# Kernel tuning notes

Measured on AMD Instinct MI355X. Metric: run time of the kernel, lower is better.

The kernel has to match this reference:

```python
import jax, jax.numpy as jnp
import numpy as np

B, L, D = 32, 512, 384
T_MAX = 4096
PAD_VALUE = 0.0
EXPAND_SCALE = 1.0


def setup_inputs() -> dict:
    key = jax.random.key(0)
    k1, k2, k3 = jax.random.split(key, 3)
    sequence = jax.random.normal(k1, (B, L, D), dtype=jnp.float32)
    duration = jax.random.randint(k2, (B, L), 0, 8, dtype=jnp.int64)
    padding_mask = jax.random.randint(k3, (B, L), 0, 2) == 1
    return {"sequence": sequence, "duration": duration,
            "padding_mask": padding_mask, "max_length": T_MAX}


def reference(sequence, duration, padding_mask, max_length):
    # expanded_duration = round(expand_scale * duration)
    exp_dur = jnp.round(EXPAND_SCALE * duration.astype(jnp.float32)).astype(jnp.int32)
    # mask padded tokens in the input sequence with pad_value
    seq = jnp.where(padding_mask[..., None], PAD_VALUE, sequence)  # (B, L, D)
    # cumulative durations: token t occupies output slots [cum[t-1], cum[t])
    cum = jnp.cumsum(exp_dur, axis=1)  # (B, L)
    pos = jnp.arange(max_length, dtype=cum.dtype)  # (T,)
    # idx[b, j] = first token index whose cumulative end exceeds j
    idx = jax.vmap(lambda c: jnp.searchsorted(c, pos, side="right"))(cum)  # (B, T)
    valid = pos[None, :] < cum[:, -1:]  # (B, T): within total expanded length
    idx = jnp.clip(idx, 0, seq.shape[1] - 1)
    out = jnp.take_along_axis(seq, idx[..., None], axis=1)  # (B, T, D)
    out = jnp.where(valid[..., None], out, PAD_VALUE)
    return out, exp_dur
```

## Files before the change

kernel.cpp:

```cpp
#include <hip/hip_runtime.h>

constexpr int B = 32;
constexpr int L = 512;
constexpr int D = 384;
constexpr int T = 4096;
constexpr int VPR = D / 4;
constexpr int OUT0 = B * T * D;
constexpr int RPB = 16;
constexpr int BLOCKS_PER_BATCH = T / RPB;
constexpr int NBLK = B * BLOCKS_PER_BATCH;
constexpr int BS = 256;
constexpr int PASSES = RPB * VPR / BS;

__global__ __launch_bounds__(L) void scan_k(const int* __restrict__ dur,
                                            int* __restrict__ cum,
                                            float* __restrict__ exp_dur_out) {
    const int b = blockIdx.x;
    const int t = threadIdx.x;
    __shared__ int s[L];
    int d = dur[b * L + t];
    exp_dur_out[b * L + t] = (float)d;
    s[t] = d;
    __syncthreads();
    #pragma unroll
    for (int off = 1; off < L; off <<= 1) {
        int v = (t >= off) ? s[t - off] : 0;
        __syncthreads();
        s[t] += v;
        __syncthreads();
    }
    cum[b * L + t] = s[t];
}

__global__ __launch_bounds__(BS) void fused_k(const float4* __restrict__ seq,
                                              const int* __restrict__ cum,
                                              const int* __restrict__ mask,
                                              float4* __restrict__ out) {
    __shared__ int s_cum[L];
    __shared__ int s_src[RPB];

    const int blk   = blockIdx.x;
    const int b     = blk >> 8;
    const int chunk = blk & 255;
    const int row0  = chunk * RPB;
    const int tid   = threadIdx.x;

    #pragma unroll
    for (int i = 0; i < L / BS; ++i)
        s_cum[i * BS + tid] = cum[b * L + i * BS + tid];
    __syncthreads();

    if (tid < RPB) {
        const int j = row0 + tid;
        const int total = s_cum[L - 1];
        int res = -1;
        if (j < total) {
            int lo = 0, hi = L;
            while (lo < hi) {
                int mid = (lo + hi) >> 1;
                if (s_cum[mid] <= j) lo = mid + 1; else hi = mid;
            }
            res = mask[b * L + lo] ? -1 : (b * L + lo);
        }
        s_src[tid] = res;
    }
    __syncthreads();

    float4* obase = out + (size_t)(b * T + row0) * VPR;
    #pragma unroll
    for (int p = 0; p < PASSES; ++p) {
        const int idx = p * BS + tid;
        const int r   = idx / VPR;
        const int col = idx - r * VPR;
        const int s   = s_src[r];
        float4 v = make_float4(0.f, 0.f, 0.f, 0.f);
        if (s >= 0) v = seq[(size_t)s * VPR + col];
        obase[idx] = v;
    }
}

extern "C" void kernel_launch(void* const* d_in, const int* in_sizes, int n_in,
                              void* d_out, int out_size, void* d_ws, size_t ws_size,
                              hipStream_t stream) {
    const float* seq  = (const float*)d_in[0];
    const int*   dur  = (const int*)d_in[1];
    const int*   mask = (const int*)d_in[2];

    float* out      = (float*)d_out;
    float* expd_out = out + OUT0;

    int* cum = (int*)d_ws;

    scan_k<<<B, L, 0, stream>>>(dur, cum, expd_out);
    fused_k<<<NBLK, BS, 0, stream>>>((const float4*)seq, cum, mask,
                                     (float4*)out);
}
```

Before: 218.1 us.

## Precompute per-row source map by scatter; use nontemporal stores in copy kernel

The scan kernel now scatters each token's global source index into a per-output-row map in workspace, with -1 marking padded or out-of-range rows. This replaces the per-block cumsum load and binary search. The copy kernel reads that map directly, drops its shared memory and barriers, and writes output with nontemporal stores to avoid polluting the cache. The trade-off is a serial scatter loop in the small kernel (up to 7 writes per thread) plus extra map writes and reads.

```diff
diff --git a/kernel.cpp b/kernel.cpp
--- a/kernel.cpp
+++ b/kernel.cpp
@@ -12,14 +12,17 @@
 constexpr int BS = 256;
 constexpr int PASSES = RPB * VPR / BS;
 
-__global__ __launch_bounds__(L) void scan_k(const int* __restrict__ dur,
-                                            int* __restrict__ cum,
-                                            float* __restrict__ exp_dur_out) {
+typedef float f32x4 __attribute__((ext_vector_type(4)));
+
+__global__ __launch_bounds__(L) void map_k(const int* __restrict__ dur,
+                                           const int* __restrict__ mask,
+                                           int* __restrict__ srcmap,
+                                           float* __restrict__ expd) {
     const int b = blockIdx.x;
     const int t = threadIdx.x;
     __shared__ int s[L];
     int d = dur[b * L + t];
-    exp_dur_out[b * L + t] = (float)d;
+    expd[b * L + t] = (float)d;
     s[t] = d;
     __syncthreads();
     #pragma unroll
@@ -29,53 +32,40 @@
         s[t] += v;
         __syncthreads();
     }
-    cum[b * L + t] = s[t];
+    const int end = s[t];
+
+    int4* m4 = (int4*)(srcmap + b * T);
+    m4[t * 2 + 0] = make_int4(-1, -1, -1, -1);
+    m4[t * 2 + 1] = make_int4(-1, -1, -1, -1);
+    __syncthreads();
+
+    if (d > 0 && !mask[b * L + t]) {
+        const int src = b * L + t;
+        int* m = srcmap + b * T;
+        for (int k = end - d; k < end; ++k) m[k] = src;
+    }
 }
 
-__global__ __launch_bounds__(BS) void fused_k(const float4* __restrict__ seq,
-                                              const int* __restrict__ cum,
-                                              const int* __restrict__ mask,
-                                              float4* __restrict__ out) {
-    __shared__ int s_cum[L];
-    __shared__ int s_src[RPB];
+__global__ __launch_bounds__(BS) void copy_k(const f32x4* __restrict__ seq,
+                                             const int* __restrict__ srcmap,
+                                             f32x4* __restrict__ out) {
+    const int blk  = blockIdx.x;
+    const int b    = blk >> 8;
+    const int row0 = (blk & 255) * RPB;
+    const int tid  = threadIdx.x;
 
-    const int blk   = blockIdx.x;
-    const int b     = blk >> 8;
-    const int chunk = blk & 255;
-    const int row0  = chunk * RPB;
-    const int tid   = threadIdx.x;
+    const int* __restrict__ m = srcmap + b * T + row0;
+    f32x4* obase = out + (size_t)(b * T + row0) * VPR;
 
-    #pragma unroll
-    for (int i = 0; i < L / BS; ++i)
-        s_cum[i * BS + tid] = cum[b * L + i * BS + tid];
-    __syncthreads();
-
-    if (tid < RPB) {
-        const int j = row0 + tid;
-        const int total = s_cum[L - 1];
-        int res = -1;
-        if (j < total) {
-            int lo = 0, hi = L;
-            while (lo < hi) {
-                int mid = (lo + hi) >> 1;
-                if (s_cum[mid] <= j) lo = mid + 1; else hi = mid;
-            }
-            res = mask[b * L + lo] ? -1 : (b * L + lo);
-        }
-        s_src[tid] = res;
-    }
-    __syncthreads();
-
-    float4* obase = out + (size_t)(b * T + row0) * VPR;
     #pragma unroll
     for (int p = 0; p < PASSES; ++p) {
         const int idx = p * BS + tid;
         const int r   = idx / VPR;
         const int col = idx - r * VPR;
-        const int s   = s_src[r];
-        float4 v = make_float4(0.f, 0.f, 0.f, 0.f);
+        const int s   = m[r];
+        f32x4 v = {0.f, 0.f, 0.f, 0.f};
         if (s >= 0) v = seq[(size_t)s * VPR + col];
-        obase[idx] = v;
+        __builtin_nontemporal_store(v, obase + idx);
     }
 }
 
@@ -89,9 +79,8 @@
     float* out      = (float*)d_out;
     float* expd_out = out + OUT0;
 
-    int* cum = (int*)d_ws;
+    int* srcmap = (int*)d_ws;
 
-    scan_k<<<B, L, 0, stream>>>(dur, cum, expd_out);
-    fused_k<<<NBLK, BS, 0, stream>>>((const float4*)seq, cum, mask,
-                                     (float4*)out);
+    map_k<<<B, L, 0, stream>>>(dur, mask, srcmap, expd_out);
+    copy_k<<<NBLK, BS, 0, stream>>>((const f32x4*)seq, srcmap, (f32x4*)out);
 }
```

New measurement: 230.7 us. +5.8%, slower.
